# Optimization experiments

Hardware: AMD Instinct MI355X
Metric: run time of the kernel (lower is better)

## Reference

```python
import jax, jax.numpy as jnp
import numpy as np

N = 512   # memory_units == batch (module broadcasting requires B == N)
M = 256   # memory_unit_size
A = 128   # action_size
HS = 512  # hidden_size
C = 512   # controller_size


def setup_inputs() -> dict:
    key = jax.random.key(0)
    ks = jax.random.split(key, 20)
    s = 0.02  # small init keeps softplus(gamma)~0.7 so w**gamma stays stable
    d = {
        'action': jax.random.normal(ks[0], (N, A), jnp.float32),
        'hidden_state': jax.random.normal(ks[1], (N, HS), jnp.float32),
        'prev_read_weight': jax.random.uniform(ks[2], (N, N), jnp.float32),
        'prev_write_weight': jax.random.uniform(ks[3], (N, N), jnp.float32),
        'memory': jax.random.normal(ks[4], (N, M), jnp.float32),
        # GRU (single layer, single step, h0 = 0)
        'W_ih': jax.random.normal(ks[5], (3 * C, A + HS), jnp.float32) * s,
        'W_hh': jax.random.normal(ks[6], (3 * C, C), jnp.float32) * s,
        'b_ih': jnp.zeros((3 * C,), jnp.float32),
        'b_hh': jnp.zeros((3 * C,), jnp.float32),
        # heads
        'W_read': jax.random.normal(ks[7], (M, C), jnp.float32) * s,
        'b_read': jnp.zeros((M,), jnp.float32),
        'W_write': jax.random.normal(ks[8], (M, C), jnp.float32) * s,
        'b_write': jnp.zeros((M,), jnp.float32),
        'W_shift': jax.random.normal(ks[9], (N, C), jnp.float32) * s,
        'b_shift': jnp.zeros((N,), jnp.float32),
        'W_gamma': jax.random.normal(ks[10], (1, C), jnp.float32) * s,
        'b_gamma': jnp.zeros((1,), jnp.float32),
        'W_gate': jax.random.normal(ks[11], (1, C), jnp.float32) * s,
        'b_gate': jnp.zeros((1,), jnp.float32),
    }
    return d


def _lin(x, W, b):
    return x @ W.T + b


def _content_weight(key, memory):
    # cosine similarity then softmax over dim=1 (the batch/column axis),
    # exactly as in the torch source
    k = key / (jnp.linalg.norm(key, axis=1, keepdims=True) + 1e-16)
    m = memory / (jnp.linalg.norm(memory, axis=1, keepdims=True) + 1e-16)
    sim = m @ k.T  # [N, B]
    return jax.nn.softmax(sim, axis=1)


def reference(action, hidden_state, prev_read_weight, prev_write_weight, memory,
              W_ih, W_hh, b_ih, b_hh,
              W_read, b_read, W_write, b_write,
              W_shift, b_shift, W_gamma, b_gamma, W_gate, b_gate):
    # ---- GRU, one step, h0 = 0 (so h @ W_hh = 0, only b_hh contributes) ----
    x = jnp.concatenate([action, hidden_state], axis=1)      # [B, A+HS]
    gi = x @ W_ih.T + b_ih                                    # [B, 3C]
    gr, gz, gn = jnp.split(gi, 3, axis=1)
    hr, hz, hn = jnp.split(b_hh, 3)
    r = jax.nn.sigmoid(gr + hr)
    z = jax.nn.sigmoid(gz + hz)
    n = jnp.tanh(gn + r * hn)
    h = (1.0 - z) * n                                         # controller_out [B, C]

    # ---- content addressing ----
    read_key = _lin(h, W_read, b_read)                        # [B, M]
    write_key = _lin(h, W_write, b_write)
    rw = _content_weight(read_key, memory)                    # [N, B]
    ww = _content_weight(write_key, memory)

    # ---- interpolation gate (broadcast [B,1] against [N,B], valid since B==N) ----
    g = jax.nn.sigmoid(_lin(h, W_gate, b_gate))               # [B, 1]
    rw = g * rw + (1.0 - g) * prev_read_weight
    ww = g * ww + (1.0 - g) * prev_write_weight

    # ---- circular convolution: result[i,b] = sum_j w[(i-j)%N, b] * s[j, b] ----
    shift = jax.nn.softmax(_lin(h, W_shift, b_shift), axis=1)  # [B, N]
    ar = jnp.arange(N)
    idx = (ar[:, None] - ar[None, :]) % N                      # [N, N] circulant index

    def circ(w):
        return jnp.einsum('ijb,jb->ib', w[idx], shift)         # [N, B]

    # ---- sharpen: w ** gamma (gamma [B,1] broadcast, B==N), normalize over dim 0 ----
    gamma = jax.nn.softplus(_lin(h, W_gamma, b_gamma))         # [B, 1]

    def sharpen(w):
        wp = w ** gamma
        return wp / jnp.sum(wp, axis=0, keepdims=True)

    rw = sharpen(circ(rw))
    ww = sharpen(circ(ww))

    read_vector = rw @ memory                                  # [N, M] (pre-write memory)
    return (read_vector, rw, ww)
```

## Files before the change

### kernel.cpp

```cpp
#include <hip/hip_runtime.h>
#include <math.h>

#define N   512
#define M   256
#define A   128
#define HS  512
#define C   512

#define WS_H       0
#define WS_HEADS   262144
#define WS_SIMR    786432
#define WS_SIMW    1048576
#define WS_SHIFT   1310720
#define WS_WGRT    1572864
#define WS_WGWT    1835008
#define WS_SHIFTT  2097152
#define WS_CIRCTR  2359296
#define WS_CIRCTW  2621440
#define WS_MEMT    2883584
#define WS_G       3014656
#define WS_GAMMA   3015168
#define WS_INVM    3015680
#define WS_INVKR   3016192
#define WS_INVKW   3016704
#define WS_CSR     3017216
#define WS_CSW     3017728

#define LD4(p) (*reinterpret_cast<const float4*>(p))
#define LD2(p) (*reinterpret_cast<const float2*>(p))

typedef short bf16x8 __attribute__((ext_vector_type(8)));
typedef float f32x16 __attribute__((ext_vector_type(16)));

struct HiLo { bf16x8 hi, lo; };

__device__ __forceinline__ HiLo split8(const float4 u, const float4 v) {
  const float x[8] = {u.x, u.y, u.z, u.w, v.x, v.y, v.z, v.w};
  union { unsigned int w[4]; bf16x8 v; } H, L;
#pragma unroll
  for (int d = 0; d < 4; ++d) {
    const unsigned int a = __float_as_uint(x[2 * d]);
    const unsigned int b = __float_as_uint(x[2 * d + 1]);
    H.w[d] = (a >> 16) | (b & 0xFFFF0000u);
    const float la = x[2 * d]     - __uint_as_float(a & 0xFFFF0000u);
    const float lb = x[2 * d + 1] - __uint_as_float(b & 0xFFFF0000u);
    L.w[d] = (__float_as_uint(la) >> 16) | (__float_as_uint(lb) & 0xFFFF0000u);
  }
  HiLo r; r.hi = H.v; r.lo = L.v;
  return r;
}

__device__ __forceinline__ f32x16 mm3(const HiLo& a, const HiLo& b, f32x16 acc) {
  acc = __builtin_amdgcn_mfma_f32_32x32x16_bf16(a.hi, b.hi, acc, 0, 0, 0);
  acc = __builtin_amdgcn_mfma_f32_32x32x16_bf16(a.hi, b.lo, acc, 0, 0, 0);
  acc = __builtin_amdgcn_mfma_f32_32x32x16_bf16(a.lo, b.hi, acc, 0, 0, 0);
  return acc;
}

template <int NK>
__device__ __forceinline__ f32x16 mfma_tile(const float* __restrict__ Abase, int lda,
                                            const float* __restrict__ Bbase, int ldb,
                                            int lane) {
  const int m = lane & 31, koff = (lane >> 5) * 8;
  const float* pa = Abase + m * lda + koff;
  const float* pb = Bbase + m * ldb + koff;
  f32x16 acc;
#pragma unroll
  for (int t = 0; t < 16; ++t) acc[t] = 0.0f;
  float4 na0 = LD4(pa), na1 = LD4(pa + 4);
  float4 nb0 = LD4(pb), nb1 = LD4(pb + 4);
#pragma unroll 4
  for (int ks = 0; ks < NK; ++ks) {
    const float4 ca0 = na0, ca1 = na1, cb0 = nb0, cb1 = nb1;
    if (ks + 1 < NK) {
      const int k = (ks + 1) * 16;
      na0 = LD4(pa + k); na1 = LD4(pa + k + 4);
      nb0 = LD4(pb + k); nb1 = LD4(pb + k + 4);
    }
    const HiLo Af = split8(ca0, ca1);
    const HiLo Bf = split8(cb0, cb1);
    acc = mm3(Af, Bf, acc);
  }
  return acc;
}

#define ACC_ROW(t, lane) (((t) & 3) + 8 * ((t) >> 2) + 4 * ((lane) >> 5))

__global__ __launch_bounds__(64) void k_gruh(const float* __restrict__ action,
                                             const float* __restrict__ hidden,
                                             const float* __restrict__ W_ih,
                                             const float* __restrict__ b_ih,
                                             const float* __restrict__ b_hh,
                                             float* __restrict__ h) {
  const int lane = threadIdx.x;
  const int r0 = blockIdx.x * 32, c0 = blockIdx.y * 32;
  const int m = lane & 31, koff = (lane >> 5) * 8;
  const float* pa_act = action + (r0 + m) * 128 + koff;
  const float* pa_hid = hidden + (r0 + m) * 512 + koff;
  const float* pR = W_ih + (c0 + m) * 640 + koff;
  const float* pZ = pR + 512 * 640;
  const float* pN = pZ + 512 * 640;

  f32x16 aR, aZ, aN;
#pragma unroll
  for (int t = 0; t < 16; ++t) { aR[t] = 0.f; aZ[t] = 0.f; aN[t] = 0.f; }

  float4 na0 = LD4(pa_act), na1 = LD4(pa_act + 4);
  float4 nr0 = LD4(pR), nr1 = LD4(pR + 4);
  float4 nz0 = LD4(pZ), nz1 = LD4(pZ + 4);
  float4 nn0 = LD4(pN), nn1 = LD4(pN + 4);
#pragma unroll 4
  for (int ks = 0; ks < 40; ++ks) {
    const float4 ca0 = na0, ca1 = na1;
    const float4 cr0 = nr0, cr1 = nr1, cz0 = nz0, cz1 = nz1, cn0 = nn0, cn1 = nn1;
    if (ks < 39) {
      const int k = (ks + 1) * 16;
      const float* pa = (k < 128) ? (pa_act + k) : (pa_hid + (k - 128));
      na0 = LD4(pa); na1 = LD4(pa + 4);
      nr0 = LD4(pR + k); nr1 = LD4(pR + k + 4);
      nz0 = LD4(pZ + k); nz1 = LD4(pZ + k + 4);
      nn0 = LD4(pN + k); nn1 = LD4(pN + k + 4);
    }
    const HiLo Af = split8(ca0, ca1);
    const HiLo Rf = split8(cr0, cr1);
    const HiLo Zf = split8(cz0, cz1);
    const HiLo Nf = split8(cn0, cn1);
    aR = mm3(Af, Rf, aR);
    aZ = mm3(Af, Zf, aZ);
    aN = mm3(Af, Nf, aN);
  }

  const int col = c0 + m;
  const float br = b_ih[col] + b_hh[col];
  const float bz = b_ih[512 + col] + b_hh[512 + col];
  const float bn = b_ih[1024 + col];
  const float hn = b_hh[1024 + col];
#pragma unroll
  for (int t = 0; t < 16; ++t) {
    const int row = r0 + ACC_ROW(t, lane);
    const float gr = aR[t] + br, gz = aZ[t] + bz, gn = aN[t] + bn;
    const float rr = 1.0f / (1.0f + expf(-gr));
    const float zz = 1.0f / (1.0f + expf(-gz));
    h[row * 512 + col] = (1.0f - zz) * tanhf(gn + rr * hn);
  }
}

__global__ __launch_bounds__(64) void k_heads(const float* __restrict__ h,
                                              const float* __restrict__ W_read, const float* __restrict__ b_read,
                                              const float* __restrict__ W_write, const float* __restrict__ b_write,
                                              const float* __restrict__ W_shift, const float* __restrict__ b_shift,
                                              float* __restrict__ heads) {
  const int lane = threadIdx.x;
  const int r0 = blockIdx.x * 32;
  const int n0 = blockIdx.y * 32;
  const float* W;
  const float* bias;
  if (n0 < 256)      { W = W_read  + n0 * 512;         bias = b_read  + n0; }
  else if (n0 < 512) { W = W_write + (n0 - 256) * 512; bias = b_write + (n0 - 256); }
  else               { W = W_shift + (n0 - 512) * 512; bias = b_shift + (n0 - 512); }

  const f32x16 acc = mfma_tile<32>(h + r0 * 512, 512, W, 512, lane);
  const int col = lane & 31;
  const float bv = bias[col];
#pragma unroll
  for (int t = 0; t < 16; ++t)
    heads[(r0 + ACC_ROW(t, lane)) * 1024 + n0 + col] = acc[t] + bv;
}

__global__ __launch_bounds__(64) void k_ggnorms(const float* __restrict__ h,
                                                const float* __restrict__ W_gate, const float* __restrict__ b_gate,
                                                const float* __restrict__ W_gamma, const float* __restrict__ b_gamma,
                                                const float* __restrict__ memory,
                                                const float* __restrict__ heads,
                                                float* __restrict__ g, float* __restrict__ gamma,
                                                float* __restrict__ invm, float* __restrict__ invkr,
                                                float* __restrict__ invkw) {
  const int r = blockIdx.x, t = threadIdx.x;
  if (r < 512) {
    float ag = 0.f, am = 0.f;
#pragma unroll
    for (int u = 0; u < 8; ++u) {
      const float hv = h[r * 512 + t + 64 * u];
      ag = fmaf(hv, W_gate[t + 64 * u], ag);
      am = fmaf(hv, W_gamma[t + 64 * u], am);
    }
    for (int o = 32; o > 0; o >>= 1) { ag += __shfl_down(ag, o); am += __shfl_down(am, o); }
    if (t == 0) {
      g[r] = 1.0f / (1.0f + expf(-(ag + b_gate[0])));
      const float x = am + b_gamma[0];
      gamma[r] = (x > 0.f) ? (x + log1pf(expf(-x))) : log1pf(expf(x));
    }
    return;
  }
  float ss;
  float* dst;
  if (r < 1024) {
    const float4 v = LD4(memory + (r - 512) * 256 + t * 4);
    ss = v.x * v.x + v.y * v.y + v.z * v.z + v.w * v.w;
    dst = invm + (r - 512);
  } else {
    const int row = (r < 1536) ? (r - 1024) : (r - 1536);
    const int seg = (r < 1536) ? 0 : 256;
    const float4 v = LD4(heads + row * 1024 + seg + t * 4);
    ss = v.x * v.x + v.y * v.y + v.z * v.z + v.w * v.w;
    dst = ((r < 1536) ? invkr : invkw) + row;
  }
  for (int o = 32; o > 0; o >>= 1) ss += __shfl_down(ss, o);
  if (t == 0) *dst = 1.0f / (sqrtf(ss) + 1e-16f);
}

__global__ __launch_bounds__(64) void k_sim(const float* __restrict__ memory,
                                            const float* __restrict__ heads,
                                            float* __restrict__ simR, float* __restrict__ simW) {
  const int lane = threadIdx.x;
  const int i0 = blockIdx.x * 32;
  const int b0 = blockIdx.y * 32;
  const int seg = blockIdx.z ? 256 : 0;
  float* out = blockIdx.z ? simW : simR;
  const f32x16 acc = mfma_tile<16>(memory + i0 * 256, 256,
                                   heads + b0 * 1024 + seg, 1024, lane);
  const int col = lane & 31;
#pragma unroll
  for (int t = 0; t < 16; ++t)
    out[(i0 + ACC_ROW(t, lane)) * 512 + b0 + col] = acc[t];
}

__global__ __launch_bounds__(256) void k_rowsoft(const float* __restrict__ simR, const float* __restrict__ simW,
                                                 const float* __restrict__ heads,
                                                 const float* __restrict__ invm, const float* __restrict__ invkr,
                                                 const float* __restrict__ invkw, const float* __restrict__ g,
                                                 const float* __restrict__ prevR, const float* __restrict__ prevW,
                                                 float* __restrict__ wgr, float* __restrict__ wgw,
                                                 float* __restrict__ shift_nat) {
  __shared__ float red[8];
  const int row = blockIdx.x, mode = blockIdx.y, t = threadIdx.x;
  float v0, v1;
  if (mode == 2) {
    const float2 s = LD2(heads + row * 1024 + 512 + 2 * t);
    v0 = s.x; v1 = s.y;
  } else {
    const float* sim = mode ? simW : simR;
    const float* invk = mode ? invkw : invkr;
    const float2 s = LD2(sim + row * 512 + 2 * t);
    const float sc = invm[row];
    v0 = s.x * sc * invk[2 * t];
    v1 = s.y * sc * invk[2 * t + 1];
  }
  float mx = fmaxf(v0, v1);
  for (int o = 32; o > 0; o >>= 1) mx = fmaxf(mx, __shfl_down(mx, o));
  if ((t & 63) == 0) red[t >> 6] = mx;
  __syncthreads();
  mx = fmaxf(fmaxf(red[0], red[1]), fmaxf(red[2], red[3]));
  const float e0 = expf(v0 - mx), e1 = expf(v1 - mx);
  float s2 = e0 + e1;
  for (int o = 32; o > 0; o >>= 1) s2 += __shfl_down(s2, o);
  if ((t & 63) == 0) red[4 + (t >> 6)] = s2;
  __syncthreads();
  const float S = (red[4] + red[5]) + (red[6] + red[7]);
  const float inv = 1.0f / S;
  const float p0 = e0 * inv, p1 = e1 * inv;
  if (mode == 2) {
    *reinterpret_cast<float2*>(shift_nat + row * 512 + 2 * t) = make_float2(p0, p1);
  } else {
    const float* prev = mode ? prevW : prevR;
    float* outw = mode ? wgw : wgr;
    const float gv = g[row];
    const float2 pr = LD2(prev + row * 512 + 2 * t);
    *reinterpret_cast<float2*>(outw + row * 512 + 2 * t) =
        make_float2(gv * p0 + (1.0f - gv) * pr.x, gv * p1 + (1.0f - gv) * pr.y);
  }
}

__global__ __launch_bounds__(256) void k_transpose(const float* __restrict__ wgr, const float* __restrict__ wgw,
                                                   const float* __restrict__ shift_nat,
                                                   float* __restrict__ wgrT, float* __restrict__ wgwT,
                                                   float* __restrict__ shiftT) {
  __shared__ float tile[32][33];
  const int z = blockIdx.z;
  const float* src = (z == 0) ? wgr : (z == 1) ? wgw : shift_nat;
  float* dst = (z == 0) ? wgrT : (z == 1) ? wgwT : shiftT;
  const int bx = blockIdx.x, by = blockIdx.y, tx = threadIdx.x, ty = threadIdx.y;
#pragma unroll
  for (int k2 = 0; k2 < 4; ++k2)
    tile[ty + 8 * k2][tx] = src[(by * 32 + ty + 8 * k2) * 512 + bx * 32 + tx];
  __syncthreads();
#pragma unroll
  for (int k2 = 0; k2 < 4; ++k2)
    dst[(bx * 32 + ty + 8 * k2) * 512 + by * 32 + tx] = tile[tx][ty + 8 * k2];
}

__global__ __launch_bounds__(256) void k_memT(const float* __restrict__ mem, float* __restrict__ memT) {
  __shared__ float tile[32][33];
  const int bx = blockIdx.x, by = blockIdx.y, tx = threadIdx.x, ty = threadIdx.y;
#pragma unroll
  for (int k2 = 0; k2 < 4; ++k2)
    tile[ty + 8 * k2][tx] = mem[(by * 32 + ty + 8 * k2) * 256 + bx * 32 + tx];
  __syncthreads();
#pragma unroll
  for (int k2 = 0; k2 < 4; ++k2)
    memT[(bx * 32 + ty + 8 * k2) * 512 + by * 32 + tx] = tile[tx][ty + 8 * k2];
}

__global__ __launch_bounds__(256) void k_circ(const float* __restrict__ wgrT, const float* __restrict__ wgwT,
                                              const float* __restrict__ shiftT,
                                              const float* __restrict__ gamma,
                                              float* __restrict__ circTR, float* __restrict__ circTW,
                                              float* __restrict__ csumR, float* __restrict__ csumW) {
  __shared__ float ls[4][1600];
  const int wid = threadIdx.x >> 6, lane = threadIdx.x & 63;
  const int b = blockIdx.x * 4 + wid;
  const float* wsrc = (blockIdx.y ? wgwT : wgrT) + b * 512;
  const float* ssrc = shiftT + b * 512;
  float* out = (blockIdx.y ? circTW : circTR) + b * 512;
  float* cs = blockIdx.y ? csumW : csumR;
  float* wl = ls[wid];
  float* sl = ls[wid] + 1056;

#pragma unroll
  for (int u = 0; u < 8; ++u) {
    const int k = lane + 64 * u;
    const float v = wsrc[k];
    wl[k + (k >> 5)] = v;
    const int k2 = k + 512;
    wl[k2 + (k2 >> 5)] = v;
    sl[k] = ssrc[k];
  }
  __syncthreads();

  const int i0 = lane * 8;
  float acc[8] = {};
  float win[8];
#pragma unroll
  for (int q = 0; q < 8; ++q) {
    const int a0 = i0 + 512 + q;
    win[q] = wl[a0 + (a0 >> 5)];
  }
  for (int jb = 0; jb < 512; jb += 8) {
    const float4 sA = LD4(&sl[jb]);
    const float4 sB = LD4(&sl[jb + 4]);
    const float sv[8] = {sA.x, sA.y, sA.z, sA.w, sB.x, sB.y, sB.z, sB.w};
#pragma unroll
    for (int u = 0; u < 8; ++u) {
      const float s = sv[u];
#pragma unroll
      for (int t = 0; t < 8; ++t) acc[t] = fmaf(win[(t - u) & 7], s, acc[t]);
      const int na = i0 + 511 - (jb + u);
      win[(7 - u) & 7] = wl[na + (na >> 5)];
    }
  }
  const float4 gm0 = LD4(gamma + i0);
  const float4 gm1 = LD4(gamma + i0 + 4);
  const float ge[8] = {gm0.x, gm0.y, gm0.z, gm0.w, gm1.x, gm1.y, gm1.z, gm1.w};
  float p[8];
  float local = 0.f;
#pragma unroll
  for (int q = 0; q < 8; ++q) { p[q] = powf(acc[q], ge[q]); local += p[q]; }
  *reinterpret_cast<float4*>(out + i0) = make_float4(p[0], p[1], p[2], p[3]);
  *reinterpret_cast<float4*>(out + i0 + 4) = make_float4(p[4], p[5], p[6], p[7]);
  for (int o = 32; o > 0; o >>= 1) local += __shfl_down(local, o);
  if (lane == 0) cs[b] = local;
}

__global__ __launch_bounds__(256) void k_finalw(const float* __restrict__ circTR, const float* __restrict__ circTW,
                                                const float* __restrict__ csumR, const float* __restrict__ csumW,
                                                float* __restrict__ d_out) {
  __shared__ float tile[32][33];
  const int z = blockIdx.z;
  const float* src = z ? circTW : circTR;
  const float* cs = z ? csumW : csumR;
  float* dst = d_out + 131072 + z * 262144;
  const int bx = blockIdx.x, by = blockIdx.y, tx = threadIdx.x, ty = threadIdx.y;
#pragma unroll
  for (int k2 = 0; k2 < 4; ++k2) {
    const int r = by * 32 + ty + 8 * k2;
    tile[ty + 8 * k2][tx] = src[r * 512 + bx * 32 + tx] * (1.0f / cs[r]);
  }
  __syncthreads();
#pragma unroll
  for (int k2 = 0; k2 < 4; ++k2)
    dst[(bx * 32 + ty + 8 * k2) * 512 + by * 32 + tx] = tile[tx][ty + 8 * k2];
}

__global__ __launch_bounds__(64) void k_readvec(const float* __restrict__ rw,
                                                const float* __restrict__ memT,
                                                float* __restrict__ rv) {
  const int lane = threadIdx.x;
  const int i0 = blockIdx.x * 32;
  const int m0 = blockIdx.y * 32;
  const f32x16 acc = mfma_tile<32>(rw + i0 * 512, 512, memT + m0 * 512, 512, lane);
  const int col = lane & 31;
#pragma unroll
  for (int t = 0; t < 16; ++t)
    rv[(i0 + ACC_ROW(t, lane)) * 256 + m0 + col] = acc[t];
}

extern "C" void kernel_launch(void* const* d_in, const int* in_sizes, int n_in,
                              void* d_out, int out_size, void* d_ws, size_t ws_size,
                              hipStream_t stream) {
  const float* action  = (const float*)d_in[0];
  const float* hidden  = (const float*)d_in[1];
  const float* prevR   = (const float*)d_in[2];
  const float* prevW   = (const float*)d_in[3];
  const float* memory  = (const float*)d_in[4];
  const float* W_ih    = (const float*)d_in[5];
  const float* b_ih    = (const float*)d_in[7];
  const float* b_hh    = (const float*)d_in[8];
  const float* W_read  = (const float*)d_in[9];
  const float* b_read  = (const float*)d_in[10];
  const float* W_write = (const float*)d_in[11];
  const float* b_write = (const float*)d_in[12];
  const float* W_shift = (const float*)d_in[13];
  const float* b_shift = (const float*)d_in[14];
  const float* W_gamma = (const float*)d_in[15];
  const float* b_gamma = (const float*)d_in[16];
  const float* W_gate  = (const float*)d_in[17];
  const float* b_gate  = (const float*)d_in[18];

  float* ws = (float*)d_ws;
  float* out = (float*)d_out;

  k_memT<<<dim3(8, 16), dim3(32, 8), 0, stream>>>(memory, ws + WS_MEMT);
  k_gruh<<<dim3(16, 16), 64, 0, stream>>>(action, hidden, W_ih, b_ih, b_hh, ws + WS_H);
  k_heads<<<dim3(16, 32), 64, 0, stream>>>(ws + WS_H, W_read, b_read, W_write, b_write,
                                           W_shift, b_shift, ws + WS_HEADS);
  k_ggnorms<<<2048, 64, 0, stream>>>(ws + WS_H, W_gate, b_gate, W_gamma, b_gamma,
                                     memory, ws + WS_HEADS,
                                     ws + WS_G, ws + WS_GAMMA,
                                     ws + WS_INVM, ws + WS_INVKR, ws + WS_INVKW);
  k_sim<<<dim3(16, 16, 2), 64, 0, stream>>>(memory, ws + WS_HEADS, ws + WS_SIMR, ws + WS_SIMW);
  k_rowsoft<<<dim3(512, 3), 256, 0, stream>>>(ws + WS_SIMR, ws + WS_SIMW, ws + WS_HEADS,
                                              ws + WS_INVM, ws + WS_INVKR, ws + WS_INVKW,
                                              ws + WS_G, prevR, prevW,
                                              ws + WS_SIMR, ws + WS_SIMW, ws + WS_SHIFT);
  k_transpose<<<dim3(16, 16, 3), dim3(32, 8), 0, stream>>>(ws + WS_SIMR, ws + WS_SIMW, ws + WS_SHIFT,
                                                           ws + WS_WGRT, ws + WS_WGWT, ws + WS_SHIFTT);
  k_circ<<<dim3(128, 2), 256, 0, stream>>>(ws + WS_WGRT, ws + WS_WGWT, ws + WS_SHIFTT,
                                           ws + WS_GAMMA,
                                           ws + WS_CIRCTR, ws + WS_CIRCTW,
                                           ws + WS_CSR, ws + WS_CSW);
  k_finalw<<<dim3(16, 16, 2), dim3(32, 8), 0, stream>>>(ws + WS_CIRCTR, ws + WS_CIRCTW,
                                                        ws + WS_CSR, ws + WS_CSW, out);
  k_readvec<<<dim3(16, 8), 64, 0, stream>>>(out + 131072, ws + WS_MEMT, out);
}
```

Baseline: 179.9 us.

## Pre-split GEMM operands to bf16 hi/lo, split GRU GEMM, XCD-aware tile mapping

The fused GRU kernel is split into a pre-split pass for action/hidden, a GEMM over all 1536 gate columns, and an elementwise activation kernel. Memory is stored transposed and pre-split into bf16 hi/lo pairs. Block indices for the GEMMs are remapped so tiles are grouped per XCD, and the MFMA tile loop is double-buffered and fully unrolled. The read-vector GEMM is split-K across two blocks that combine via atomicAdd after a memset. This raises parallelism and removes repeated splitting, at the cost of extra launches and intermediate traffic.

```diff
diff --git a/kernel.cpp b/kernel.cpp
--- a/kernel.cpp
+++ b/kernel.cpp
@@ -17,7 +17,7 @@
 #define WS_SHIFTT  2097152
 #define WS_CIRCTR  2359296
 #define WS_CIRCTW  2621440
-#define WS_MEMT    2883584
+#define WS_MEMTS   2883584
 #define WS_G       3014656
 #define WS_GAMMA   3015168
 #define WS_INVM    3015680
@@ -25,6 +25,8 @@
 #define WS_INVKW   3016704
 #define WS_CSR     3017216
 #define WS_CSW     3017728
+#define WS_XS      0
+#define WS_GI      786432
 
 #define LD4(p) (*reinterpret_cast<const float4*>(p))
 #define LD2(p) (*reinterpret_cast<const float2*>(p))
@@ -50,6 +52,13 @@
   return r;
 }
 
+__device__ __forceinline__ HiLo reint8(const float4 q0, const float4 q1) {
+  HiLo r;
+  r.hi = *reinterpret_cast<const bf16x8*>(&q0);
+  r.lo = *reinterpret_cast<const bf16x8*>(&q1);
+  return r;
+}
+
 __device__ __forceinline__ f32x16 mm3(const HiLo& a, const HiLo& b, f32x16 acc) {
   acc = __builtin_amdgcn_mfma_f32_32x32x16_bf16(a.hi, b.hi, acc, 0, 0, 0);
   acc = __builtin_amdgcn_mfma_f32_32x32x16_bf16(a.hi, b.lo, acc, 0, 0, 0);
@@ -57,92 +66,125 @@
   return acc;
 }
 
-template <int NK>
-__device__ __forceinline__ f32x16 mfma_tile(const float* __restrict__ Abase, int lda,
-                                            const float* __restrict__ Bbase, int ldb,
-                                            int lane) {
+template <int NK, bool SA, bool SB>
+__device__ __forceinline__ f32x16 tileMM(const float* __restrict__ pa,
+                                         const float* __restrict__ pb) {
+  f32x16 acc;
+#pragma unroll
+  for (int t = 0; t < 16; ++t) acc[t] = 0.0f;
+  float4 aE0 = LD4(pa), aE1 = LD4(pa + 4);
+  float4 bE0 = LD4(pb), bE1 = LD4(pb + 4);
+  float4 aO0, aO1, bO0, bO1;
+  if (NK > 1) {
+    aO0 = LD4(pa + 16); aO1 = LD4(pa + 20);
+    bO0 = LD4(pb + 16); bO1 = LD4(pb + 20);
+  }
+#pragma unroll
+  for (int ks = 0; ks < NK; ++ks) {
+    HiLo Af, Bf;
+    if ((ks & 1) == 0) {
+      Af = SA ? reint8(aE0, aE1) : split8(aE0, aE1);
+      Bf = SB ? reint8(bE0, bE1) : split8(bE0, bE1);
+      if (ks + 2 < NK) {
+        const int k = (ks + 2) * 16;
+        aE0 = LD4(pa + k); aE1 = LD4(pa + k + 4);
+        bE0 = LD4(pb + k); bE1 = LD4(pb + k + 4);
+      }
+    } else {
+      Af = SA ? reint8(aO0, aO1) : split8(aO0, aO1);
+      Bf = SB ? reint8(bO0, bO1) : split8(bO0, bO1);
+      if (ks + 2 < NK) {
+        const int k = (ks + 2) * 16;
+        aO0 = LD4(pa + k); aO1 = LD4(pa + k + 4);
+        bO0 = LD4(pb + k); bO1 = LD4(pb + k + 4);
+      }
+    }
+    acc = mm3(Af, Bf, acc);
+  }
+  return acc;
+}
+
+#define ACC_ROW(t, lane) (((t) & 3) + 8 * ((t) >> 2) + 4 * ((lane) >> 5))
+
+__global__ __launch_bounds__(256) void k_prep(const float* __restrict__ action,
+                                              const float* __restrict__ hidden,
+                                              float* __restrict__ xs) {
+  const int idx = blockIdx.x * 256 + threadIdx.x;
+  const int row = idx / 80, g = idx % 80;
+  const float* src = (g < 16) ? (action + row * 128 + g * 8)
+                              : (hidden + row * 512 + (g - 16) * 8);
+  const HiLo s = split8(LD4(src), LD4(src + 4));
+  *reinterpret_cast<float4*>(xs + idx * 8)     = *reinterpret_cast<const float4*>(&s.hi);
+  *reinterpret_cast<float4*>(xs + idx * 8 + 4) = *reinterpret_cast<const float4*>(&s.lo);
+}
+
+__global__ __launch_bounds__(256) void k_memT(const float* __restrict__ mem,
+                                              float* __restrict__ memTs) {
+  __shared__ float tile[32][33];
+  const int bx = blockIdx.x, by = blockIdx.y, tx = threadIdx.x, ty = threadIdx.y;
+#pragma unroll
+  for (int k2 = 0; k2 < 4; ++k2)
+    tile[ty + 8 * k2][tx] = mem[(by * 32 + ty + 8 * k2) * 256 + bx * 32 + tx];
+  __syncthreads();
+  if (ty < 4) {
+    float4 q0, q1;
+    q0.x = tile[8 * ty + 0][tx]; q0.y = tile[8 * ty + 1][tx];
+    q0.z = tile[8 * ty + 2][tx]; q0.w = tile[8 * ty + 3][tx];
+    q1.x = tile[8 * ty + 4][tx]; q1.y = tile[8 * ty + 5][tx];
+    q1.z = tile[8 * ty + 6][tx]; q1.w = tile[8 * ty + 7][tx];
+    const HiLo s = split8(q0, q1);
+    float* dst = memTs + (bx * 32 + tx) * 512 + (by * 4 + ty) * 8;
+    *reinterpret_cast<float4*>(dst)     = *reinterpret_cast<const float4*>(&s.hi);
+    *reinterpret_cast<float4*>(dst + 4) = *reinterpret_cast<const float4*>(&s.lo);
+  }
+}
+
+__global__ __launch_bounds__(64) void k_ggemm(const float* __restrict__ xs,
+                                              const float* __restrict__ W_ih,
+                                              float* __restrict__ gi) {
+  const int lane = threadIdx.x;
+  const int wg = blockIdx.x;
+  const int xcd = wg & 7, inner = wg >> 3;
+  const int bi = inner & 15;
+  const int bc = xcd * 6 + (inner >> 4);
+  const int r0 = bi * 32, c0 = bc * 32;
   const int m = lane & 31, koff = (lane >> 5) * 8;
-  const float* pa = Abase + m * lda + koff;
-  const float* pb = Bbase + m * ldb + koff;
-  f32x16 acc;
-#pragma unroll
-  for (int t = 0; t < 16; ++t) acc[t] = 0.0f;
-  float4 na0 = LD4(pa), na1 = LD4(pa + 4);
-  float4 nb0 = LD4(pb), nb1 = LD4(pb + 4);
-#pragma unroll 4
-  for (int ks = 0; ks < NK; ++ks) {
-    const float4 ca0 = na0, ca1 = na1, cb0 = nb0, cb1 = nb1;
-    if (ks + 1 < NK) {
-      const int k = (ks + 1) * 16;
-      na0 = LD4(pa + k); na1 = LD4(pa + k + 4);
-      nb0 = LD4(pb + k); nb1 = LD4(pb + k + 4);
-    }
-    const HiLo Af = split8(ca0, ca1);
-    const HiLo Bf = split8(cb0, cb1);
-    acc = mm3(Af, Bf, acc);
-  }
-  return acc;
-}
-
-#define ACC_ROW(t, lane) (((t) & 3) + 8 * ((t) >> 2) + 4 * ((lane) >> 5))
-
-__global__ __launch_bounds__(64) void k_gruh(const float* __restrict__ action,
-                                             const float* __restrict__ hidden,
-                                             const float* __restrict__ W_ih,
+  const f32x16 acc = tileMM<40, true, false>(xs + (r0 + m) * 640 + koff,
+                                             W_ih + (c0 + m) * 640 + koff);
+  const int col = c0 + m;
+#pragma unroll
+  for (int t = 0; t < 16; ++t)
+    gi[(r0 + ACC_ROW(t, lane)) * 1536 + col] = acc[t];
+}
+
+__global__ __launch_bounds__(256) void k_act(const float* __restrict__ gi,
                                              const float* __restrict__ b_ih,
                                              const float* __restrict__ b_hh,
                                              float* __restrict__ h) {
-  const int lane = threadIdx.x;
-  const int r0 = blockIdx.x * 32, c0 = blockIdx.y * 32;
-  const int m = lane & 31, koff = (lane >> 5) * 8;
-  const float* pa_act = action + (r0 + m) * 128 + koff;
-  const float* pa_hid = hidden + (r0 + m) * 512 + koff;
-  const float* pR = W_ih + (c0 + m) * 640 + koff;
-  const float* pZ = pR + 512 * 640;
-  const float* pN = pZ + 512 * 640;
-
-  f32x16 aR, aZ, aN;
-#pragma unroll
-  for (int t = 0; t < 16; ++t) { aR[t] = 0.f; aZ[t] = 0.f; aN[t] = 0.f; }
-
-  float4 na0 = LD4(pa_act), na1 = LD4(pa_act + 4);
-  float4 nr0 = LD4(pR), nr1 = LD4(pR + 4);
-  float4 nz0 = LD4(pZ), nz1 = LD4(pZ + 4);
-  float4 nn0 = LD4(pN), nn1 = LD4(pN + 4);
-#pragma unroll 4
-  for (int ks = 0; ks < 40; ++ks) {
-    const float4 ca0 = na0, ca1 = na1;
-    const float4 cr0 = nr0, cr1 = nr1, cz0 = nz0, cz1 = nz1, cn0 = nn0, cn1 = nn1;
-    if (ks < 39) {
-      const int k = (ks + 1) * 16;
-      const float* pa = (k < 128) ? (pa_act + k) : (pa_hid + (k - 128));
-      na0 = LD4(pa); na1 = LD4(pa + 4);
-      nr0 = LD4(pR + k); nr1 = LD4(pR + k + 4);
-      nz0 = LD4(pZ + k); nz1 = LD4(pZ + k + 4);
-      nn0 = LD4(pN + k); nn1 = LD4(pN + k + 4);
-    }
-    const HiLo Af = split8(ca0, ca1);
-    const HiLo Rf = split8(cr0, cr1);
-    const HiLo Zf = split8(cz0, cz1);
-    const HiLo Nf = split8(cn0, cn1);
-    aR = mm3(Af, Rf, aR);
-    aZ = mm3(Af, Zf, aZ);
-    aN = mm3(Af, Nf, aN);
-  }
-
-  const int col = c0 + m;
-  const float br = b_ih[col] + b_hh[col];
-  const float bz = b_ih[512 + col] + b_hh[512 + col];
-  const float bn = b_ih[1024 + col];
-  const float hn = b_hh[1024 + col];
-#pragma unroll
-  for (int t = 0; t < 16; ++t) {
-    const int row = r0 + ACC_ROW(t, lane);
-    const float gr = aR[t] + br, gz = aZ[t] + bz, gn = aN[t] + bn;
-    const float rr = 1.0f / (1.0f + expf(-gr));
-    const float zz = 1.0f / (1.0f + expf(-gz));
-    h[row * 512 + col] = (1.0f - zz) * tanhf(gn + rr * hn);
-  }
+  const int idx = blockIdx.x * 256 + threadIdx.x;
+  const int b = idx >> 7, c4 = (idx & 127) * 4;
+  const float4 g0 = LD4(gi + b * 1536 + c4);
+  const float4 g1 = LD4(gi + b * 1536 + 512 + c4);
+  const float4 g2 = LD4(gi + b * 1536 + 1024 + c4);
+  const float4 bi0 = LD4(b_ih + c4);
+  const float4 bi1 = LD4(b_ih + 512 + c4);
+  const float4 bi2 = LD4(b_ih + 1024 + c4);
+  const float4 bh0 = LD4(b_hh + c4);
+  const float4 bh1 = LD4(b_hh + 512 + c4);
+  const float4 bh2 = LD4(b_hh + 1024 + c4);
+  const float gr[4] = {g0.x + bi0.x + bh0.x, g0.y + bi0.y + bh0.y, g0.z + bi0.z + bh0.z, g0.w + bi0.w + bh0.w};
+  const float gz[4] = {g1.x + bi1.x + bh1.x, g1.y + bi1.y + bh1.y, g1.z + bi1.z + bh1.z, g1.w + bi1.w + bh1.w};
+  const float gn[4] = {g2.x + bi2.x, g2.y + bi2.y, g2.z + bi2.z, g2.w + bi2.w};
+  const float hn[4] = {bh2.x, bh2.y, bh2.z, bh2.w};
+  float res[4];
+#pragma unroll
+  for (int u = 0; u < 4; ++u) {
+    const float r = 1.0f / (1.0f + expf(-gr[u]));
+    const float z = 1.0f / (1.0f + expf(-gz[u]));
+    res[u] = (1.0f - z) * tanhf(gn[u] + r * hn[u]);
+  }
+  float4 o; o.x = res[0]; o.y = res[1]; o.z = res[2]; o.w = res[3];
+  *reinterpret_cast<float4*>(h + b * 512 + c4) = o;
 }
 
 __global__ __launch_bounds__(64) void k_heads(const float* __restrict__ h,
@@ -151,15 +193,19 @@
                                               const float* __restrict__ W_shift, const float* __restrict__ b_shift,
                                               float* __restrict__ heads) {
   const int lane = threadIdx.x;
-  const int r0 = blockIdx.x * 32;
-  const int n0 = blockIdx.y * 32;
+  const int wg = blockIdx.x;
+  const int xcd = wg & 7, inner = wg >> 3;
+  const int bi = inner & 15;
+  const int bn = xcd * 4 + (inner >> 4);
+  const int r0 = bi * 32, n0 = bn * 32;
   const float* W;
   const float* bias;
   if (n0 < 256)      { W = W_read  + n0 * 512;         bias = b_read  + n0; }
   else if (n0 < 512) { W = W_write + (n0 - 256) * 512; bias = b_write + (n0 - 256); }
   else               { W = W_shift + (n0 - 512) * 512; bias = b_shift + (n0 - 512); }
-
-  const f32x16 acc = mfma_tile<32>(h + r0 * 512, 512, W, 512, lane);
+  const int m = lane & 31, koff = (lane >> 5) * 8;
+  const f32x16 acc = tileMM<32, false, false>(h + (r0 + m) * 512 + koff,
+                                              W + m * 512 + koff);
   const int col = lane & 31;
   const float bv = bias[col];
 #pragma unroll
@@ -217,8 +263,9 @@
   const int b0 = blockIdx.y * 32;
   const int seg = blockIdx.z ? 256 : 0;
   float* out = blockIdx.z ? simW : simR;
-  const f32x16 acc = mfma_tile<16>(memory + i0 * 256, 256,
-                                   heads + b0 * 1024 + seg, 1024, lane);
+  const int m = lane & 31, koff = (lane >> 5) * 8;
+  const f32x16 acc = tileMM<16, false, false>(memory + (i0 + m) * 256 + koff,
+                                              heads + (b0 + m) * 1024 + seg + koff);
   const int col = lane & 31;
 #pragma unroll
   for (int t = 0; t < 16; ++t)
@@ -289,18 +336,6 @@
     dst[(bx * 32 + ty + 8 * k2) * 512 + by * 32 + tx] = tile[tx][ty + 8 * k2];
 }
 
-__global__ __launch_bounds__(256) void k_memT(const float* __restrict__ mem, float* __restrict__ memT) {
-  __shared__ float tile[32][33];
-  const int bx = blockIdx.x, by = blockIdx.y, tx = threadIdx.x, ty = threadIdx.y;
-#pragma unroll
-  for (int k2 = 0; k2 < 4; ++k2)
-    tile[ty + 8 * k2][tx] = mem[(by * 32 + ty + 8 * k2) * 256 + bx * 32 + tx];
-  __syncthreads();
-#pragma unroll
-  for (int k2 = 0; k2 < 4; ++k2)
-    memT[(bx * 32 + ty + 8 * k2) * 512 + by * 32 + tx] = tile[tx][ty + 8 * k2];
-}
-
 __global__ __launch_bounds__(256) void k_circ(const float* __restrict__ wgrT, const float* __restrict__ wgwT,
                                               const float* __restrict__ shiftT,
                                               const float* __restrict__ gamma,
@@ -382,16 +417,19 @@
 }
 
 __global__ __launch_bounds__(64) void k_readvec(const float* __restrict__ rw,
-                                                const float* __restrict__ memT,
+                                                const float* __restrict__ memTs,
                                                 float* __restrict__ rv) {
   const int lane = threadIdx.x;
   const int i0 = blockIdx.x * 32;
   const int m0 = blockIdx.y * 32;
-  const f32x16 acc = mfma_tile<32>(rw + i0 * 512, 512, memT + m0 * 512, 512, lane);
+  const int kz = blockIdx.z * 256;
+  const int m = lane & 31, koff = (lane >> 5) * 8;
+  const f32x16 acc = tileMM<16, false, true>(rw + (i0 + m) * 512 + kz + koff,
+                                             memTs + (m0 + m) * 512 + kz + koff);
   const int col = lane & 31;
 #pragma unroll
   for (int t = 0; t < 16; ++t)
-    rv[(i0 + ACC_ROW(t, lane)) * 256 + m0 + col] = acc[t];
+    atomicAdd(&rv[(i0 + ACC_ROW(t, lane)) * 256 + m0 + col], acc[t]);
 }
 
 extern "C" void kernel_launch(void* const* d_in, const int* in_sizes, int n_in,
@@ -419,10 +457,14 @@
   float* ws = (float*)d_ws;
   float* out = (float*)d_out;
 
-  k_memT<<<dim3(8, 16), dim3(32, 8), 0, stream>>>(memory, ws + WS_MEMT);
-  k_gruh<<<dim3(16, 16), 64, 0, stream>>>(action, hidden, W_ih, b_ih, b_hh, ws + WS_H);
-  k_heads<<<dim3(16, 32), 64, 0, stream>>>(ws + WS_H, W_read, b_read, W_write, b_write,
-                                           W_shift, b_shift, ws + WS_HEADS);
+  hipMemsetAsync(out, 0, 131072 * sizeof(float), stream);
+
+  k_prep<<<160, 256, 0, stream>>>(action, hidden, ws + WS_XS);
+  k_memT<<<dim3(8, 16), dim3(32, 8), 0, stream>>>(memory, ws + WS_MEMTS);
+  k_ggemm<<<768, 64, 0, stream>>>(ws + WS_XS, W_ih, ws + WS_GI);
+  k_act<<<256, 256, 0, stream>>>(ws + WS_GI, b_ih, b_hh, ws + WS_H);
+  k_heads<<<512, 64, 0, stream>>>(ws + WS_H, W_read, b_read, W_write, b_write,
+                                  W_shift, b_shift, ws + WS_HEADS);
   k_ggnorms<<<2048, 64, 0, stream>>>(ws + WS_H, W_gate, b_gate, W_gamma, b_gamma,
                                      memory, ws + WS_HEADS,
                                      ws + WS_G, ws + WS_GAMMA,
@@ -440,5 +482,5 @@
                                            ws + WS_CSR, ws + WS_CSW);
   k_finalw<<<dim3(16, 16, 2), dim3(32, 8), 0, stream>>>(ws + WS_CIRCTR, ws + WS_CIRCTW,
                                                         ws + WS_CSR, ws + WS_CSW, out);
-  k_readvec<<<dim3(16, 8), 64, 0, stream>>>(out + 131072, ws + WS_MEMT, out);
-}
+  k_readvec<<<dim3(16, 8, 2), 64, 0, stream>>>(out + 131072, ws + WS_MEMTS, out);
+}
```

Result: slower. 183.5 us (+2.0%).
